# Kernel optimization log

Hardware: AMD Instinct MI355X
Metric: run time of the kernel (lower is better)

The kernel has to match this reference:

```python
import jax, jax.numpy as jnp
import numpy as np

TEMPERATURE = 1.0  # config['attention_temperature']


def setup_inputs() -> dict:
    key = jax.random.key(0)
    k1, k2, k3 = jax.random.split(key, 3)
    B, S, F, D = 4, 4096, 33, 64
    x = jax.random.normal(k1, (B, S, F), dtype=jnp.float32)
    Wq = jax.random.normal(k2, (F, D), dtype=jnp.float32) / np.sqrt(F)
    bq = jnp.zeros((D,), dtype=jnp.float32)
    Wk = jax.random.normal(k3, (F, D), dtype=jnp.float32) / np.sqrt(F)
    bk = jnp.zeros((D,), dtype=jnp.float32)
    return {"x": x, "Wq": Wq, "bq": bq, "Wk": Wk, "bk": bk}


def reference(x, Wq, bq, Wk, bk):
    # queries/keys: affine projections of the same input (MLP with one layer)
    q = x @ Wq + bq                              # [B, S, D]
    k = x @ Wk + bk                              # [B, S, D]
    qkt = jnp.einsum("bsd,btd->bst", q, k)       # [B, S, S]
    # non-standard normalization: divide each row by its max, scale by temperature
    row_max = jnp.max(qkt, axis=-1, keepdims=True)
    dist = jax.nn.softmax(TEMPERATURE * qkt / row_max, axis=-1)
    return dist
```

## Files before the change

kernel.cpp:

```cpp
#include <hip/hip_runtime.h>
#include <hip/hip_bf16.h>

typedef __bf16 bf16_t;
typedef __bf16 bf16x8 __attribute__((ext_vector_type(8)));
typedef float f32x4 __attribute__((ext_vector_type(4)));
typedef __fp16 f16x2 __attribute__((ext_vector_type(2)));

#define BATCH 4
#define SEQ 4096
#define FIN 33
#define DIM 64
#define LOG2E 1.4426950408889634f
#define NWAVE 16
#define NTILE 16

__device__ __forceinline__ float dexp2(float x) { return __builtin_amdgcn_exp2f(x); }

__global__ __launch_bounds__(256) void qk_proj_kernel(
    const float* __restrict__ x, const float* __restrict__ Wq,
    const float* __restrict__ bq, const float* __restrict__ Wk,
    const float* __restrict__ bk,
    bf16_t* __restrict__ qout, bf16_t* __restrict__ kout)
{
    __shared__ float sWq[FIN * DIM];
    __shared__ float sWk[FIN * DIM];
    __shared__ float sb[2 * DIM];
    const int t = threadIdx.x;
    for (int i = t; i < FIN * DIM; i += 256) { sWq[i] = Wq[i]; sWk[i] = Wk[i]; }
    if (t < DIM) { sb[t] = bq[t]; sb[DIM + t] = bk[t]; }
    __syncthreads();

    const int row = blockIdx.x * 4 + (t >> 6);
    const int d   = t & 63;
    const float* xr = x + (size_t)row * FIN;
    float qacc = sb[d], kacc = sb[DIM + d];
#pragma unroll
    for (int f = 0; f < FIN; ++f) {
        const float xv = xr[f];
        qacc += xv * sWq[f * DIM + d];
        kacc += xv * sWk[f * DIM + d];
    }
    qout[(size_t)row * DIM + d] = (bf16_t)qacc;
    kout[(size_t)row * DIM + d] = (bf16_t)kacc;
}


__device__ __forceinline__ f32x4 mm2(bf16x8 a0, bf16x8 a1, bf16x8 b0, bf16x8 b1)
{
    f32x4 acc = {0.f, 0.f, 0.f, 0.f};
    acc = __builtin_amdgcn_mfma_f32_16x16x32_bf16(a0, b0, acc, 0, 0, 0);
    acc = __builtin_amdgcn_mfma_f32_16x16x32_bf16(a1, b1, acc, 0, 0, 0);
    return acc;
}

#define LD(ct, h) (*reinterpret_cast<const bf16x8*>(kw + (size_t)(ct) * 16 * DIM + (h) * 32))

__global__ __launch_bounds__(1024, 4) void attn_kernel(
    const bf16_t* __restrict__ qg, const bf16_t* __restrict__ kg,
    float* __restrict__ out)
{
    const int wg  = blockIdx.x;
    const int b   = wg >> 8;
    const int r0  = (wg & 255) << 4;
    const int t   = threadIdx.x;
    const int w   = t >> 6;
    const int l   = t & 63;
    const int lr  = l & 15;
    const int kg4 = l >> 4;

    const bf16_t* qbase = qg + (size_t)(b * SEQ + r0) * DIM;
    const bf16_t* kbase = kg + (size_t)b * SEQ * DIM;

    const bf16x8 a0 = *reinterpret_cast<const bf16x8*>(qbase + lr * DIM + kg4 * 8);
    const bf16x8 a1 = *reinterpret_cast<const bf16x8*>(qbase + lr * DIM + 32 + kg4 * 8);

    const int col0 = w << 8;
    const bf16_t* kw = kbase + (size_t)(col0 + lr) * DIM + kg4 * 8;

    __shared__ float redM[NWAVE][16];
    __shared__ float redZ[NWAVE][16];

    f16x2 s[NTILE][2];

    float vmax[4] = {-3.4e38f, -3.4e38f, -3.4e38f, -3.4e38f};
    {
        bf16x8 p0a = LD(0, 0), p0b = LD(0, 1);
        bf16x8 p1a = LD(1, 0), p1b = LD(1, 1);
#pragma unroll
        for (int ct = 0; ct < NTILE; ct += 2) {
            f32x4 acc0 = mm2(a0, a1, p0a, p0b);
            if (ct + 2 < NTILE) { p0a = LD(ct + 2, 0); p0b = LD(ct + 2, 1); }
#pragma unroll
            for (int j = 0; j < 4; ++j) vmax[j] = fmaxf(vmax[j], acc0[j]);
            s[ct][0] = __builtin_amdgcn_cvt_pkrtz(acc0[0], acc0[1]);
            s[ct][1] = __builtin_amdgcn_cvt_pkrtz(acc0[2], acc0[3]);

            f32x4 acc1 = mm2(a0, a1, p1a, p1b);
            if (ct + 3 < NTILE) { p1a = LD(ct + 3, 0); p1b = LD(ct + 3, 1); }
#pragma unroll
            for (int j = 0; j < 4; ++j) vmax[j] = fmaxf(vmax[j], acc1[j]);
            s[ct + 1][0] = __builtin_amdgcn_cvt_pkrtz(acc1[0], acc1[1]);
            s[ct + 1][1] = __builtin_amdgcn_cvt_pkrtz(acc1[2], acc1[3]);
        }
    }
#pragma unroll
    for (int m = 1; m < 16; m <<= 1) {
#pragma unroll
        for (int j = 0; j < 4; ++j) vmax[j] = fmaxf(vmax[j], __shfl_xor(vmax[j], m, 64));
    }
    if (lr == 0) {
#pragma unroll
        for (int j = 0; j < 4; ++j) redM[w][kg4 * 4 + j] = vmax[j];
    }
    __syncthreads();
    float cM[4];
#pragma unroll
    for (int j = 0; j < 4; ++j) {
        const int r = kg4 * 4 + j;
        float m = redM[0][r];
#pragma unroll
        for (int ww = 1; ww < NWAVE; ++ww) m = fmaxf(m, redM[ww][r]);
        cM[j] = LOG2E / m;
    }

    float vsum[4] = {0.f, 0.f, 0.f, 0.f};
#pragma unroll
    for (int ct = 0; ct < NTILE; ++ct) {
#pragma unroll
        for (int h = 0; h < 2; ++h) {
            const float e0 = dexp2(fmaf((float)s[ct][h][0], cM[2 * h + 0], -LOG2E));
            const float e1 = dexp2(fmaf((float)s[ct][h][1], cM[2 * h + 1], -LOG2E));
            vsum[2 * h + 0] += e0;
            vsum[2 * h + 1] += e1;
            s[ct][h] = __builtin_amdgcn_cvt_pkrtz(e0, e1);
        }
    }
#pragma unroll
    for (int m = 1; m < 16; m <<= 1) {
#pragma unroll
        for (int j = 0; j < 4; ++j) vsum[j] += __shfl_xor(vsum[j], m, 64);
    }
    if (lr == 0) {
#pragma unroll
        for (int j = 0; j < 4; ++j) redZ[w][kg4 * 4 + j] = vsum[j];
    }
    __syncthreads();
    float invZ[4];
#pragma unroll
    for (int j = 0; j < 4; ++j) {
        const int r = kg4 * 4 + j;
        float z = redZ[0][r];
#pragma unroll
        for (int ww = 1; ww < NWAVE; ++ww) z += redZ[ww][r];
        invZ[j] = 1.0f / z;
    }

    float* orow = out + (size_t)(b * SEQ + r0 + kg4 * 4) * SEQ + col0 + lr;
#pragma unroll
    for (int ct = 0; ct < NTILE; ++ct) {
#pragma unroll
        for (int h = 0; h < 2; ++h) {
            orow[(size_t)(2 * h + 0) * SEQ + ct * 16] = (float)s[ct][h][0] * invZ[2 * h + 0];
            orow[(size_t)(2 * h + 1) * SEQ + ct * 16] = (float)s[ct][h][1] * invZ[2 * h + 1];
        }
    }
}

extern "C" void kernel_launch(void* const* d_in, const int* in_sizes, int n_in,
                              void* d_out, int out_size, void* d_ws, size_t ws_size,
                              hipStream_t stream)
{
    const float* x  = (const float*)d_in[0];
    const float* Wq = (const float*)d_in[1];
    const float* bq = (const float*)d_in[2];
    const float* Wk = (const float*)d_in[3];
    const float* bk = (const float*)d_in[4];
    float* out = (float*)d_out;

    bf16_t* qws = (bf16_t*)d_ws;
    bf16_t* kws = qws + (size_t)BATCH * SEQ * DIM;

    qk_proj_kernel<<<(BATCH * SEQ) / 4, 256, 0, stream>>>(x, Wq, bq, Wk, bk, qws, kws);
    attn_kernel<<<BATCH * (SEQ / 16), 1024, 0, stream>>>(qws, kws, out);
}
```

Before: 127.1 us.

## Make attention kernel persistent over four row blocks, overlapping stores with next QK^T

```diff
diff --git a/kernel.cpp b/kernel.cpp
--- a/kernel.cpp
+++ b/kernel.cpp
@@ -13,6 +13,7 @@
 #define LOG2E 1.4426950408889634f
 #define NWAVE 16
 #define NTILE 16
+#define NBLK 4
 
 __device__ __forceinline__ float dexp2(float x) { return __builtin_amdgcn_exp2f(x); }
 
@@ -59,31 +60,86 @@
     const bf16_t* __restrict__ qg, const bf16_t* __restrict__ kg,
     float* __restrict__ out)
 {
-    const int wg  = blockIdx.x;
-    const int b   = wg >> 8;
-    const int r0  = (wg & 255) << 4;
-    const int t   = threadIdx.x;
-    const int w   = t >> 6;
-    const int l   = t & 63;
-    const int lr  = l & 15;
-    const int kg4 = l >> 4;
-
-    const bf16_t* qbase = qg + (size_t)(b * SEQ + r0) * DIM;
-    const bf16_t* kbase = kg + (size_t)b * SEQ * DIM;
-
-    const bf16x8 a0 = *reinterpret_cast<const bf16x8*>(qbase + lr * DIM + kg4 * 8);
-    const bf16x8 a1 = *reinterpret_cast<const bf16x8*>(qbase + lr * DIM + 32 + kg4 * 8);
-
+    const int wgid = ((blockIdx.x & 7) << 5) | (blockIdx.x >> 3);
+    const int blk0 = wgid * NBLK;
+    const int b    = blk0 >> 8;
+    const int t    = threadIdx.x;
+    const int w    = t >> 6;
+    const int l    = t & 63;
+    const int lr   = l & 15;
+    const int kg4  = l >> 4;
     const int col0 = w << 8;
-    const bf16_t* kw = kbase + (size_t)(col0 + lr) * DIM + kg4 * 8;
+
+    const bf16_t* kw = kg + ((size_t)b * SEQ + col0 + lr) * DIM + kg4 * 8;
 
     __shared__ float redM[NWAVE][16];
     __shared__ float redZ[NWAVE][16];
 
     f16x2 s[NTILE][2];
-
-    float vmax[4] = {-3.4e38f, -3.4e38f, -3.4e38f, -3.4e38f};
+    float cM[4], invZ[4];
+
+#define REDUCE_M(vmax)                                                          \
+    {                                                                           \
+        _Pragma("unroll")                                                       \
+        for (int m = 1; m < 16; m <<= 1) {                                      \
+            _Pragma("unroll")                                                   \
+            for (int j = 0; j < 4; ++j)                                         \
+                vmax[j] = fmaxf(vmax[j], __shfl_xor(vmax[j], m, 64));           \
+        }                                                                       \
+        if (lr == 0) {                                                          \
+            _Pragma("unroll")                                                   \
+            for (int j = 0; j < 4; ++j) redM[w][kg4 * 4 + j] = vmax[j];         \
+        }                                                                       \
+        __syncthreads();                                                        \
+        _Pragma("unroll")                                                       \
+        for (int j = 0; j < 4; ++j) {                                           \
+            const int r = kg4 * 4 + j;                                          \
+            float mm = redM[0][r];                                              \
+            _Pragma("unroll")                                                   \
+            for (int ww = 1; ww < NWAVE; ++ww) mm = fmaxf(mm, redM[ww][r]);     \
+            cM[j] = LOG2E / mm;                                                 \
+        }                                                                       \
+    }
+
+#define PASS_B()                                                                \
+    {                                                                           \
+        float vsum[4] = {0.f, 0.f, 0.f, 0.f};                                   \
+        _Pragma("unroll")                                                       \
+        for (int ct = 0; ct < NTILE; ++ct) {                                    \
+            _Pragma("unroll")                                                   \
+            for (int h = 0; h < 2; ++h) {                                       \
+                const float e0 = dexp2(fmaf((float)s[ct][h][0], cM[2*h+0], -LOG2E)); \
+                const float e1 = dexp2(fmaf((float)s[ct][h][1], cM[2*h+1], -LOG2E)); \
+                vsum[2*h+0] += e0;                                              \
+                vsum[2*h+1] += e1;                                              \
+                s[ct][h] = __builtin_amdgcn_cvt_pkrtz(e0, e1);                  \
+            }                                                                   \
+        }                                                                       \
+        _Pragma("unroll")                                                       \
+        for (int m = 1; m < 16; m <<= 1) {                                      \
+            _Pragma("unroll")                                                   \
+            for (int j = 0; j < 4; ++j) vsum[j] += __shfl_xor(vsum[j], m, 64);  \
+        }                                                                       \
+        if (lr == 0) {                                                          \
+            _Pragma("unroll")                                                   \
+            for (int j = 0; j < 4; ++j) redZ[w][kg4 * 4 + j] = vsum[j];         \
+        }                                                                       \
+        __syncthreads();                                                        \
+        _Pragma("unroll")                                                       \
+        for (int j = 0; j < 4; ++j) {                                           \
+            const int r = kg4 * 4 + j;                                          \
+            float z = redZ[0][r];                                               \
+            _Pragma("unroll")                                                   \
+            for (int ww = 1; ww < NWAVE; ++ww) z += redZ[ww][r];                \
+            invZ[j] = 1.0f / z;                                                 \
+        }                                                                       \
+    }
+
     {
+        const bf16_t* qb = qg + (size_t)(blk0 * 16) * DIM;
+        const bf16x8 a0 = *reinterpret_cast<const bf16x8*>(qb + lr * DIM + kg4 * 8);
+        const bf16x8 a1 = *reinterpret_cast<const bf16x8*>(qb + lr * DIM + 32 + kg4 * 8);
+        float vmax[4] = {-3.4e38f, -3.4e38f, -3.4e38f, -3.4e38f};
         bf16x8 p0a = LD(0, 0), p0b = LD(0, 1);
         bf16x8 p1a = LD(1, 0), p1b = LD(1, 1);
 #pragma unroll
@@ -102,66 +158,55 @@
             s[ct + 1][0] = __builtin_amdgcn_cvt_pkrtz(acc1[0], acc1[1]);
             s[ct + 1][1] = __builtin_amdgcn_cvt_pkrtz(acc1[2], acc1[3]);
         }
-    }
-#pragma unroll
-    for (int m = 1; m < 16; m <<= 1) {
-#pragma unroll
-        for (int j = 0; j < 4; ++j) vmax[j] = fmaxf(vmax[j], __shfl_xor(vmax[j], m, 64));
-    }
-    if (lr == 0) {
-#pragma unroll
-        for (int j = 0; j < 4; ++j) redM[w][kg4 * 4 + j] = vmax[j];
-    }
-    __syncthreads();
-    float cM[4];
-#pragma unroll
-    for (int j = 0; j < 4; ++j) {
-        const int r = kg4 * 4 + j;
-        float m = redM[0][r];
-#pragma unroll
-        for (int ww = 1; ww < NWAVE; ++ww) m = fmaxf(m, redM[ww][r]);
-        cM[j] = LOG2E / m;
-    }
-
-    float vsum[4] = {0.f, 0.f, 0.f, 0.f};
-#pragma unroll
-    for (int ct = 0; ct < NTILE; ++ct) {
-#pragma unroll
-        for (int h = 0; h < 2; ++h) {
-            const float e0 = dexp2(fmaf((float)s[ct][h][0], cM[2 * h + 0], -LOG2E));
-            const float e1 = dexp2(fmaf((float)s[ct][h][1], cM[2 * h + 1], -LOG2E));
-            vsum[2 * h + 0] += e0;
-            vsum[2 * h + 1] += e1;
-            s[ct][h] = __builtin_amdgcn_cvt_pkrtz(e0, e1);
-        }
-    }
-#pragma unroll
-    for (int m = 1; m < 16; m <<= 1) {
-#pragma unroll
-        for (int j = 0; j < 4; ++j) vsum[j] += __shfl_xor(vsum[j], m, 64);
-    }
-    if (lr == 0) {
-#pragma unroll
-        for (int j = 0; j < 4; ++j) redZ[w][kg4 * 4 + j] = vsum[j];
-    }
-    __syncthreads();
-    float invZ[4];
-#pragma unroll
-    for (int j = 0; j < 4; ++j) {
-        const int r = kg4 * 4 + j;
-        float z = redZ[0][r];
-#pragma unroll
-        for (int ww = 1; ww < NWAVE; ++ww) z += redZ[ww][r];
-        invZ[j] = 1.0f / z;
-    }
-
-    float* orow = out + (size_t)(b * SEQ + r0 + kg4 * 4) * SEQ + col0 + lr;
-#pragma unroll
-    for (int ct = 0; ct < NTILE; ++ct) {
-#pragma unroll
-        for (int h = 0; h < 2; ++h) {
-            orow[(size_t)(2 * h + 0) * SEQ + ct * 16] = (float)s[ct][h][0] * invZ[2 * h + 0];
-            orow[(size_t)(2 * h + 1) * SEQ + ct * 16] = (float)s[ct][h][1] * invZ[2 * h + 1];
+        REDUCE_M(vmax);
+        PASS_B();
+    }
+
+#pragma unroll
+    for (int i = 0; i < NBLK; ++i) {
+        const int blk = blk0 + i;
+        float* orow = out + ((size_t)(blk * 16 + kg4 * 4)) * SEQ + col0 + lr;
+        if (i + 1 < NBLK) {
+            const bf16_t* qb = qg + (size_t)((blk + 1) * 16) * DIM;
+            const bf16x8 a0 = *reinterpret_cast<const bf16x8*>(qb + lr * DIM + kg4 * 8);
+            const bf16x8 a1 = *reinterpret_cast<const bf16x8*>(qb + lr * DIM + 32 + kg4 * 8);
+            float vmax[4] = {-3.4e38f, -3.4e38f, -3.4e38f, -3.4e38f};
+            bf16x8 p0a = LD(0, 0), p0b = LD(0, 1);
+            bf16x8 p1a = LD(1, 0), p1b = LD(1, 1);
+#pragma unroll
+            for (int ct = 0; ct < NTILE; ct += 2) {
+                f32x4 acc0 = mm2(a0, a1, p0a, p0b);
+                if (ct + 2 < NTILE) { p0a = LD(ct + 2, 0); p0b = LD(ct + 2, 1); }
+                orow[(size_t)0 * SEQ + ct * 16] = (float)s[ct][0][0] * invZ[0];
+                orow[(size_t)1 * SEQ + ct * 16] = (float)s[ct][0][1] * invZ[1];
+                orow[(size_t)2 * SEQ + ct * 16] = (float)s[ct][1][0] * invZ[2];
+                orow[(size_t)3 * SEQ + ct * 16] = (float)s[ct][1][1] * invZ[3];
+#pragma unroll
+                for (int j = 0; j < 4; ++j) vmax[j] = fmaxf(vmax[j], acc0[j]);
+                s[ct][0] = __builtin_amdgcn_cvt_pkrtz(acc0[0], acc0[1]);
+                s[ct][1] = __builtin_amdgcn_cvt_pkrtz(acc0[2], acc0[3]);
+
+                f32x4 acc1 = mm2(a0, a1, p1a, p1b);
+                if (ct + 3 < NTILE) { p1a = LD(ct + 3, 0); p1b = LD(ct + 3, 1); }
+                orow[(size_t)0 * SEQ + (ct + 1) * 16] = (float)s[ct + 1][0][0] * invZ[0];
+                orow[(size_t)1 * SEQ + (ct + 1) * 16] = (float)s[ct + 1][0][1] * invZ[1];
+                orow[(size_t)2 * SEQ + (ct + 1) * 16] = (float)s[ct + 1][1][0] * invZ[2];
+                orow[(size_t)3 * SEQ + (ct + 1) * 16] = (float)s[ct + 1][1][1] * invZ[3];
+#pragma unroll
+                for (int j = 0; j < 4; ++j) vmax[j] = fmaxf(vmax[j], acc1[j]);
+                s[ct + 1][0] = __builtin_amdgcn_cvt_pkrtz(acc1[0], acc1[1]);
+                s[ct + 1][1] = __builtin_amdgcn_cvt_pkrtz(acc1[2], acc1[3]);
+            }
+            REDUCE_M(vmax);
+            PASS_B();
+        } else {
+#pragma unroll
+            for (int ct = 0; ct < NTILE; ++ct) {
+                orow[(size_t)0 * SEQ + ct * 16] = (float)s[ct][0][0] * invZ[0];
+                orow[(size_t)1 * SEQ + ct * 16] = (float)s[ct][0][1] * invZ[1];
+                orow[(size_t)2 * SEQ + ct * 16] = (float)s[ct][1][0] * invZ[2];
+                orow[(size_t)3 * SEQ + ct * 16] = (float)s[ct][1][1] * invZ[3];
+            }
         }
     }
 }
@@ -181,5 +226,5 @@
     bf16_t* kws = qws + (size_t)BATCH * SEQ * DIM;
 
     qk_proj_kernel<<<(BATCH * SEQ) / 4, 256, 0, stream>>>(x, Wq, bq, Wk, bk, qws, kws);
-    attn_kernel<<<BATCH * (SEQ / 16), 1024, 0, stream>>>(qws, kws, out);
-}
+    attn_kernel<<<256, 1024, 0, stream>>>(qws, kws, out);
+}
```

New measurement: 189.9 us. 49.4% more time.
